# Kernel tuning notes

Measured on AMD Instinct MI355X. Metric: run time of the kernel, lower is better.

The kernel has to match this reference:

```python
import jax, jax.numpy as jnp
import numpy as np

B, J, D = 64, 512, 1024

def setup_inputs() -> dict:
    key = jax.random.key(0)
    k_x, k_m, k1, k2, k3 = jax.random.split(key, 5)
    x = jax.random.normal(k_x, (B, J, D), dtype=jnp.float32)
    mask = (jax.random.uniform(k_m, (B, J)) > 0.1).astype(jnp.float32)
    s1 = 1.0 / np.sqrt(D)
    W1 = jax.random.uniform(k1, (D, D), minval=-s1, maxval=s1, dtype=jnp.float32)
    b1 = jnp.zeros((D,), jnp.float32)
    W2 = jax.random.uniform(k2, (D, 1), minval=-s1, maxval=s1, dtype=jnp.float32)
    b2 = jnp.zeros((1,), jnp.float32)
    W3 = jax.random.uniform(k3, (D, 3), minval=-s1, maxval=s1, dtype=jnp.float32)
    b3 = jnp.zeros((3,), jnp.float32)
    return {"x": x, "mask": mask, "W1": W1, "b1": b1, "W2": W2, "b2": b2, "W3": W3, "b3": b3}

def reference(x, mask, W1, b1, W2, b2, W3, b3):
    # MLP attention scoring: linear1 -> tanh -> linear2 -> sigmoid
    h = jnp.tanh(jnp.einsum('bjd,de->bje', x, W1) + b1)          # [B,J,D]
    val = jax.nn.sigmoid(jnp.einsum('bjd,do->bjo', h, W2) + b2)  # [B,J,1]
    val = val * mask[:, :, None]                                  # mask out pads
    inv_sum = 1.0 / jnp.sum(val, axis=(1, 2))                     # [B]
    att_weights = val * inv_sum[:, None, None]                    # [B,J,1]
    pooled = jnp.einsum('bjk,bjm->bk', x, att_weights)            # [B,D]
    output_val = pooled @ W3 + b3                                 # [B,3]
    return output_val, att_weights
```

## Files before the change

kernel.cpp:

```cpp
#include <hip/hip_runtime.h>
#include <math.h>
#include <stdint.h>

#define B_ 64
#define J_ 512
#define D_ 1024

typedef __attribute__((ext_vector_type(8))) short short8;
typedef __attribute__((ext_vector_type(4))) float f32x4;

#define GLOBAL_AS __attribute__((address_space(1)))
#define LDS_AS    __attribute__((address_space(3)))

__device__ __forceinline__ void async16(const void* g, void* l) {
    __builtin_amdgcn_global_load_lds((const GLOBAL_AS uint32_t*)g,
                                     (LDS_AS uint32_t*)l, 16, 0, 0);
}

__device__ __forceinline__ float fast_tanh(float x) {
    return 1.0f - 2.0f / (1.0f + __expf(2.0f * x));
}

__device__ __forceinline__ unsigned short f2bf(float f) {
    uint32_t u = __builtin_bit_cast(uint32_t, f);
    u += 0x7fffu + ((u >> 16) & 1u);
    return (unsigned short)(u >> 16);
}

__device__ __forceinline__ uint32_t pk2(float a, float b) {
    return (uint32_t)f2bf(a) | ((uint32_t)f2bf(b) << 16);
}

__global__ __launch_bounds__(256) void prep_kernel(const float* __restrict__ W1,
                                                   unsigned short* __restrict__ W1t,
                                                   float* __restrict__ pooled) {
    __shared__ float t[32][33];
    const int b   = blockIdx.x;
    const int tid = threadIdx.x;
    if (b < 256) pooled[b * 256 + tid] = 0.f;
    const int bx = b & 31, by = b >> 5;
    const int tx = tid & 31, ty = tid >> 5;
    const int n = bx * 32 + tx;
    for (int i = ty; i < 32; i += 8)
        t[i][tx] = W1[(size_t)(by * 32 + i) * D_ + n];
    __syncthreads();
    const int k = by * 32 + tx;
    for (int i = ty; i < 32; i += 8)
        W1t[(size_t)(bx * 32 + i) * D_ + k] = f2bf(t[tx][i]);
}

__global__ __launch_bounds__(512, 4) void gemm_score_kernel(
    const float* __restrict__ x, const unsigned short* __restrict__ W1t,
    const float* __restrict__ b1, const float* __restrict__ W2,
    const float* __restrict__ b2, const float* __restrict__ mask,
    float* __restrict__ val_ws, float* __restrict__ pooled)
{
    __shared__ __align__(16) unsigned short ldsA[64 * 64];
    __shared__ __align__(16) unsigned short ldsB[512 * 64];

    const int tid  = threadIdx.x;
    const int wave = tid >> 6;
    const int l    = tid & 63;
    const int l15  = l & 15;
    const int kgrp = l >> 4;
    const int l7   = l & 7;
    const int r0   = blockIdx.x * 64;
    const int bb   = r0 >> 9;

    const int arow = tid >> 3;
    const int ach  = ((tid & 7) ^ (arow & 7)) << 3;
    const float* gAx = x + (size_t)(r0 + arow) * D_ + ach;

    const unsigned short* gB0 = W1t + (size_t)arow * D_ + ach;
    unsigned short* lB0 = ldsB + (wave << 9);

    int abase[2], bbase[2];
    #pragma unroll
    for (int ks = 0; ks < 2; ++ks) {
        const int swz = (((ks * 4 + kgrp) ^ l7) << 3);
        abase[ks] = l15 * 64 + swz;
        bbase[ks] = (wave * 64 + l15) * 64 + swz;
    }

    float pv[4][4];
    #pragma unroll
    for (int mi = 0; mi < 4; ++mi)
        #pragma unroll
        for (int r = 0; r < 4; ++r) pv[mi][r] = 0.f;

    uint4 curA;
    {
        const float4 p0 = *reinterpret_cast<const float4*>(gAx);
        const float4 p1 = *reinterpret_cast<const float4*>(gAx + 4);
        curA = (uint4){pk2(p0.x, p0.y), pk2(p0.z, p0.w),
                       pk2(p1.x, p1.y), pk2(p1.z, p1.w)};
    }

    #pragma unroll
    for (int n0 = 0; n0 < 2; ++n0) {
        f32x4 acc[4][4];
        #pragma unroll
        for (int mi = 0; mi < 4; ++mi)
            #pragma unroll
            for (int ni = 0; ni < 4; ++ni)
                acc[mi][ni] = (f32x4){0.f, 0.f, 0.f, 0.f};

        const size_t bofs = (size_t)n0 * 512 * D_;
        for (int k0 = 0; k0 < D_; k0 += 64) {
            *reinterpret_cast<uint4*>(ldsA + tid * 8) = curA;
            #pragma unroll
            for (int t = 0; t < 8; ++t)
                async16(gB0 + bofs + (size_t)t * 64 * D_ + k0, lB0 + t * 4096);
            __syncthreads();

            const int nk = (k0 == D_ - 64) ? 0 : k0 + 64;
            const float4 q0 = *reinterpret_cast<const float4*>(gAx + nk);
            const float4 q1 = *reinterpret_cast<const float4*>(gAx + nk + 4);

            #pragma unroll
            for (int ks = 0; ks < 2; ++ks) {
                const short8 a0 = *reinterpret_cast<const short8*>(ldsA + abase[ks]);
                const short8 a1 = *reinterpret_cast<const short8*>(ldsA + abase[ks] + 1024);
                const short8 a2 = *reinterpret_cast<const short8*>(ldsA + abase[ks] + 2048);
                const short8 a3 = *reinterpret_cast<const short8*>(ldsA + abase[ks] + 3072);
                #pragma unroll
                for (int ni = 0; ni < 4; ++ni) {
                    const short8 bv = *reinterpret_cast<const short8*>(
                        ldsB + bbase[ks] + ni * 1024);
                    acc[0][ni] = __builtin_amdgcn_mfma_f32_16x16x32_bf16(a0, bv, acc[0][ni], 0, 0, 0);
                    acc[1][ni] = __builtin_amdgcn_mfma_f32_16x16x32_bf16(a1, bv, acc[1][ni], 0, 0, 0);
                    acc[2][ni] = __builtin_amdgcn_mfma_f32_16x16x32_bf16(a2, bv, acc[2][ni], 0, 0, 0);
                    acc[3][ni] = __builtin_amdgcn_mfma_f32_16x16x32_bf16(a3, bv, acc[3][ni], 0, 0, 0);
                }
            }

            curA = (uint4){pk2(q0.x, q0.y), pk2(q0.z, q0.w),
                           pk2(q1.x, q1.y), pk2(q1.z, q1.w)};
            __syncthreads();
        }

        #pragma unroll
        for (int ni = 0; ni < 4; ++ni) {
            const int col = n0 * 512 + wave * 64 + ni * 16 + l15;
            const float b1v = b1[col];
            const float w2v = W2[col];
            #pragma unroll
            for (int mi = 0; mi < 4; ++mi)
                #pragma unroll
                for (int r = 0; r < 4; ++r) {
                    const float h = fast_tanh(acc[mi][ni][r] + b1v);
                    pv[mi][r] = fmaf(h, w2v, pv[mi][r]);
                }
        }
    }

    float* pv_part = reinterpret_cast<float*>(ldsB);
    float* vrow    = pv_part + 512;

    #pragma unroll
    for (int mi = 0; mi < 4; ++mi)
        #pragma unroll
        for (int r = 0; r < 4; ++r) {
            float s = pv[mi][r];
            s += __shfl_xor(s, 1);
            s += __shfl_xor(s, 2);
            s += __shfl_xor(s, 4);
            s += __shfl_xor(s, 8);
            if (l15 == 0) pv_part[wave * 64 + mi * 16 + kgrp * 4 + r] = s;
        }
    __syncthreads();
    if (tid < 64) {
        float s = b2[0];
        #pragma unroll
        for (int w = 0; w < 8; ++w) s += pv_part[w * 64 + tid];
        const float sg = 1.0f / (1.0f + __expf(-s));
        const float v = sg * mask[r0 + tid];
        val_ws[r0 + tid] = v;
        vrow[tid] = v;
    }
    __syncthreads();

    const int kc = tid << 1;
    float a0 = 0.f, a1 = 0.f;
    for (int row = 0; row < 64; ++row) {
        const float v = vrow[row];
        const float2 xv = *reinterpret_cast<const float2*>(
            x + (size_t)(r0 + row) * D_ + kc);
        a0 = fmaf(xv.x, v, a0);
        a1 = fmaf(xv.y, v, a1);
    }
    atomicAdd(&pooled[bb * D_ + kc], a0);
    atomicAdd(&pooled[bb * D_ + kc + 1], a1);
}

#define MT 64
#define KT 32
#define PAD 68

__global__ __launch_bounds__(256) void score_kernel_fp32(
    const float* __restrict__ x, const float* __restrict__ mask,
    const float* __restrict__ W1, const float* __restrict__ b1,
    const float* __restrict__ W2, const float* __restrict__ b2,
    float* __restrict__ val_ws, float* __restrict__ pooled)
{
    __shared__ float As[KT][PAD];
    __shared__ float Bs[KT][PAD];
    __shared__ float red[MT][17];
    __shared__ float vrow[MT];

    const int tid = threadIdx.x;
    const int tx = tid & 15;
    const int ty = tid >> 4;
    const int r0 = blockIdx.x * MT;
    const int b  = r0 >> 9;

    float pv[4] = {0.f, 0.f, 0.f, 0.f};

    for (int n0 = 0; n0 < D_; n0 += 64) {
        float acc[4][4];
        #pragma unroll
        for (int i = 0; i < 4; ++i)
            #pragma unroll
            for (int j = 0; j < 4; ++j) acc[i][j] = 0.f;

        for (int k0 = 0; k0 < D_; k0 += KT) {
            #pragma unroll
            for (int ll = 0; ll < 2; ++ll) {
                const int f   = tid + ll * 256;
                const int row = f >> 3;
                const int k4  = (f & 7) << 2;
                const float4 xv = *reinterpret_cast<const float4*>(
                    &x[(size_t)(r0 + row) * D_ + k0 + k4]);
                As[k4 + 0][row] = xv.x;
                As[k4 + 1][row] = xv.y;
                As[k4 + 2][row] = xv.z;
                As[k4 + 3][row] = xv.w;
            }
            #pragma unroll
            for (int ll = 0; ll < 2; ++ll) {
                const int f  = tid + ll * 256;
                const int k  = f >> 4;
                const int n4 = (f & 15) << 2;
                const float4 wv = *reinterpret_cast<const float4*>(
                    &W1[(size_t)(k0 + k) * D_ + n0 + n4]);
                *reinterpret_cast<float4*>(&Bs[k][n4]) = wv;
            }
            __syncthreads();
            #pragma unroll
            for (int kk = 0; kk < KT; ++kk) {
                const float4 a4 = *reinterpret_cast<const float4*>(&As[kk][ty << 2]);
                const float4 b4 = *reinterpret_cast<const float4*>(&Bs[kk][tx << 2]);
                const float av[4] = {a4.x, a4.y, a4.z, a4.w};
                const float bv[4] = {b4.x, b4.y, b4.z, b4.w};
                #pragma unroll
                for (int i = 0; i < 4; ++i)
                    #pragma unroll
                    for (int j = 0; j < 4; ++j)
                        acc[i][j] = fmaf(av[i], bv[j], acc[i][j]);
            }
            __syncthreads();
        }
        #pragma unroll
        for (int j = 0; j < 4; ++j) {
            const int col = n0 + (tx << 2) + j;
            const float b1v = b1[col];
            const float w2v = W2[col];
            #pragma unroll
            for (int i = 0; i < 4; ++i) {
                const float h = fast_tanh(acc[i][j] + b1v);
                pv[i] = fmaf(h, w2v, pv[i]);
            }
        }
    }

    #pragma unroll
    for (int i = 0; i < 4; ++i) red[(ty << 2) + i][tx] = pv[i];
    __syncthreads();

    if (tid < MT) {
        float s = 0.f;
        #pragma unroll
        for (int t = 0; t < 16; ++t) s += red[tid][t];
        const float z  = s + b2[0];
        const float sg = 1.0f / (1.0f + __expf(-z));
        const float v  = sg * mask[r0 + tid];
        val_ws[r0 + tid] = v;
        vrow[tid] = v;
    }
    __syncthreads();

    const int k = tid << 2;
    float a0 = 0.f, a1 = 0.f, a2 = 0.f, a3 = 0.f;
    for (int row = 0; row < MT; ++row) {
        const float v = vrow[row];
        const float4 xv = *reinterpret_cast<const float4*>(
            &x[(size_t)(r0 + row) * D_ + k]);
        a0 = fmaf(xv.x, v, a0);
        a1 = fmaf(xv.y, v, a1);
        a2 = fmaf(xv.z, v, a2);
        a3 = fmaf(xv.w, v, a3);
    }
    float* pb = &pooled[b * D_ + k];
    atomicAdd(pb + 0, a0);
    atomicAdd(pb + 1, a1);
    atomicAdd(pb + 2, a2);
    atomicAdd(pb + 3, a3);
}

__global__ __launch_bounds__(256) void finalize_kernel(
    const float* __restrict__ val_ws, const float* __restrict__ pooled,
    const float* __restrict__ W3, const float* __restrict__ b3,
    float* __restrict__ out)
{
    __shared__ float sred[256];
    const int b = blockIdx.x;
    const int tid = threadIdx.x;

    const float v0 = val_ws[b * J_ + tid];
    const float v1 = val_ws[b * J_ + 256 + tid];
    sred[tid] = v0 + v1;
    __syncthreads();
    for (int s = 128; s > 0; s >>= 1) {
        if (tid < s) sred[tid] += sred[tid + s];
        __syncthreads();
    }
    const float inv = 1.0f / sred[0];

    out[192 + b * J_ + tid]       = v0 * inv;
    out[192 + b * J_ + 256 + tid] = v1 * inv;

    const int k = tid << 2;
    float acc3[3] = {0.f, 0.f, 0.f};
    #pragma unroll
    for (int c = 0; c < 4; ++c) {
        const float p = pooled[b * D_ + k + c] * inv;
        acc3[0] = fmaf(p, W3[(k + c) * 3 + 0], acc3[0]);
        acc3[1] = fmaf(p, W3[(k + c) * 3 + 1], acc3[1]);
        acc3[2] = fmaf(p, W3[(k + c) * 3 + 2], acc3[2]);
    }
    for (int o = 0; o < 3; ++o) {
        __syncthreads();
        sred[tid] = acc3[o];
        __syncthreads();
        for (int s = 128; s > 0; s >>= 1) {
            if (tid < s) sred[tid] += sred[tid + s];
            __syncthreads();
        }
        if (tid == 0) out[b * 3 + o] = sred[0] + b3[o];
    }
}

extern "C" void kernel_launch(void* const* d_in, const int* in_sizes, int n_in,
                              void* d_out, int out_size, void* d_ws, size_t ws_size,
                              hipStream_t stream) {
    const float* x    = (const float*)d_in[0];
    const float* mask = (const float*)d_in[1];
    const float* W1   = (const float*)d_in[2];
    const float* b1   = (const float*)d_in[3];
    const float* W2   = (const float*)d_in[4];
    const float* b2   = (const float*)d_in[5];
    const float* W3   = (const float*)d_in[6];
    const float* b3   = (const float*)d_in[7];
    float* out = (float*)d_out;

    const size_t W1T_BYTES  = (size_t)D_ * D_ * 2;
    const size_t VAL_BYTES  = (size_t)B_ * J_ * 4;
    const size_t POOL_BYTES = (size_t)B_ * D_ * 4;
    const size_t NEED = W1T_BYTES + VAL_BYTES + POOL_BYTES;

    if (ws_size >= NEED) {
        unsigned short* W1t = (unsigned short*)d_ws;
        float* val_ws = (float*)((char*)d_ws + W1T_BYTES);
        float* pooled = (float*)((char*)d_ws + W1T_BYTES + VAL_BYTES);

        prep_kernel<<<1024, 256, 0, stream>>>(W1, W1t, pooled);
        gemm_score_kernel<<<512, 512, 0, stream>>>(x, W1t, b1, W2, b2, mask,
                                                   val_ws, pooled);
        finalize_kernel<<<B_, 256, 0, stream>>>(val_ws, pooled, W3, b3, out);
    } else {
        float* val_ws = (float*)d_ws;
        float* pooled = val_ws + B_ * J_;
        hipMemsetAsync(pooled, 0, POOL_BYTES, stream);
        score_kernel_fp32<<<(B_ * J_) / MT, 256, 0, stream>>>(
            x, mask, W1, b1, W2, b2, val_ws, pooled);
        finalize_kernel<<<B_, 256, 0, stream>>>(val_ws, pooled, W3, b3, out);
    }
}
```

Baseline: 308.1 us.

## Stream fp32 A tiles via async LDS loads and convert to bf16 after LDS read

The x tile is no longer loaded into registers, converted to bf16 and stored to LDS. It is now copied as fp32 straight into LDS with global_load_lds, using an XOR-swizzled layout. Each wave then reads fp32 from LDS and converts it with the hardware v_cvt_pk_bf16_f32 instruction just before the MFMAs. This removes the register staging and the software rounding. The cost is twice the LDS footprint and read traffic for A, repeated conversion work across waves, and the loss of the explicit register prefetch overlap for A.

```diff
diff --git a/kernel.cpp b/kernel.cpp
--- a/kernel.cpp
+++ b/kernel.cpp
@@ -27,8 +27,15 @@
     return (unsigned short)(u >> 16);
 }
 
-__device__ __forceinline__ uint32_t pk2(float a, float b) {
-    return (uint32_t)f2bf(a) | ((uint32_t)f2bf(b) << 16);
+__device__ __forceinline__ short8 cvt8(const f32x4 lo, const f32x4 hi) {
+    uint32_t w0, w1, w2, w3;
+    asm("v_cvt_pk_bf16_f32 %0, %1, %2" : "=v"(w0) : "v"(lo[0]), "v"(lo[1]));
+    asm("v_cvt_pk_bf16_f32 %0, %1, %2" : "=v"(w1) : "v"(lo[2]), "v"(lo[3]));
+    asm("v_cvt_pk_bf16_f32 %0, %1, %2" : "=v"(w2) : "v"(hi[0]), "v"(hi[1]));
+    asm("v_cvt_pk_bf16_f32 %0, %1, %2" : "=v"(w3) : "v"(hi[2]), "v"(hi[3]));
+    union { uint32_t u[4]; short8 s; } cv;
+    cv.u[0] = w0; cv.u[1] = w1; cv.u[2] = w2; cv.u[3] = w3;
+    return cv.s;
 }
 
 __global__ __launch_bounds__(256) void prep_kernel(const float* __restrict__ W1,
@@ -55,7 +62,7 @@
     const float* __restrict__ b2, const float* __restrict__ mask,
     float* __restrict__ val_ws, float* __restrict__ pooled)
 {
-    __shared__ __align__(16) unsigned short ldsA[64 * 64];
+    __shared__ __align__(16) float          ldsAf[64 * 64];
     __shared__ __align__(16) unsigned short ldsB[512 * 64];
 
     const int tid  = threadIdx.x;
@@ -67,20 +74,28 @@
     const int r0   = blockIdx.x * 64;
     const int bb   = r0 >> 9;
 
-    const int arow = tid >> 3;
-    const int ach  = ((tid & 7) ^ (arow & 7)) << 3;
-    const float* gAx = x + (size_t)(r0 + arow) * D_ + ach;
-
-    const unsigned short* gB0 = W1t + (size_t)arow * D_ + ach;
+    const int q0r = tid >> 4,          q0c = tid & 15;
+    const int q1r = (tid + 512) >> 4,  q1c = tid & 15;
+    const float* gA0 = x + (size_t)(r0 + q0r) * D_ + ((q0c ^ (q0r & 15)) << 2);
+    const float* gA1 = x + (size_t)(r0 + q1r) * D_ + ((q1c ^ (q1r & 15)) << 2);
+    float* lA0 = ldsAf + (wave << 8);
+    float* lA1 = lA0 + 2048;
+
+    const int brow = tid >> 3;
+    const int bch  = ((tid & 7) ^ (brow & 7)) << 3;
+    const unsigned short* gB0 = W1t + (size_t)brow * D_ + bch;
     unsigned short* lB0 = ldsB + (wave << 9);
 
-    int abase[2], bbase[2];
-    #pragma unroll
-    for (int ks = 0; ks < 2; ++ks) {
-        const int swz = (((ks * 4 + kgrp) ^ l7) << 3);
-        abase[ks] = l15 * 64 + swz;
-        bbase[ks] = (wave * 64 + l15) * 64 + swz;
-    }
+    int afo[4][2];
+    #pragma unroll
+    for (int mi = 0; mi < 4; ++mi)
+        #pragma unroll
+        for (int ks = 0; ks < 2; ++ks)
+            afo[mi][ks] = (mi * 16 + l15) * 64 + (((ks * 8 + kgrp * 2) ^ l15) << 2);
+    int bbase[2];
+    #pragma unroll
+    for (int ks = 0; ks < 2; ++ks)
+        bbase[ks] = (wave * 64 + l15) * 64 + (((ks * 4 + kgrp) ^ l7) << 3);
 
     float pv[4][4];
     #pragma unroll
@@ -88,15 +103,6 @@
         #pragma unroll
         for (int r = 0; r < 4; ++r) pv[mi][r] = 0.f;
 
-    uint4 curA;
-    {
-        const float4 p0 = *reinterpret_cast<const float4*>(gAx);
-        const float4 p1 = *reinterpret_cast<const float4*>(gAx + 4);
-        curA = (uint4){pk2(p0.x, p0.y), pk2(p0.z, p0.w),
-                       pk2(p1.x, p1.y), pk2(p1.z, p1.w)};
-    }
-
-    #pragma unroll
     for (int n0 = 0; n0 < 2; ++n0) {
         f32x4 acc[4][4];
         #pragma unroll
@@ -107,35 +113,31 @@
 
         const size_t bofs = (size_t)n0 * 512 * D_;
         for (int k0 = 0; k0 < D_; k0 += 64) {
-            *reinterpret_cast<uint4*>(ldsA + tid * 8) = curA;
+            async16(gA0 + k0, lA0);
+            async16(gA1 + k0, lA1);
             #pragma unroll
             for (int t = 0; t < 8; ++t)
                 async16(gB0 + bofs + (size_t)t * 64 * D_ + k0, lB0 + t * 4096);
             __syncthreads();
-
-            const int nk = (k0 == D_ - 64) ? 0 : k0 + 64;
-            const float4 q0 = *reinterpret_cast<const float4*>(gAx + nk);
-            const float4 q1 = *reinterpret_cast<const float4*>(gAx + nk + 4);
-
             #pragma unroll
             for (int ks = 0; ks < 2; ++ks) {
-                const short8 a0 = *reinterpret_cast<const short8*>(ldsA + abase[ks]);
-                const short8 a1 = *reinterpret_cast<const short8*>(ldsA + abase[ks] + 1024);
-                const short8 a2 = *reinterpret_cast<const short8*>(ldsA + abase[ks] + 2048);
-                const short8 a3 = *reinterpret_cast<const short8*>(ldsA + abase[ks] + 3072);
+                short8 a[4];
+                #pragma unroll
+                for (int mi = 0; mi < 4; ++mi) {
+                    const f32x4 lo = *reinterpret_cast<const f32x4*>(ldsAf + afo[mi][ks]);
+                    const f32x4 hi = *reinterpret_cast<const f32x4*>(ldsAf + (afo[mi][ks] ^ 4));
+                    a[mi] = cvt8(lo, hi);
+                }
                 #pragma unroll
                 for (int ni = 0; ni < 4; ++ni) {
                     const short8 bv = *reinterpret_cast<const short8*>(
                         ldsB + bbase[ks] + ni * 1024);
-                    acc[0][ni] = __builtin_amdgcn_mfma_f32_16x16x32_bf16(a0, bv, acc[0][ni], 0, 0, 0);
-                    acc[1][ni] = __builtin_amdgcn_mfma_f32_16x16x32_bf16(a1, bv, acc[1][ni], 0, 0, 0);
-                    acc[2][ni] = __builtin_amdgcn_mfma_f32_16x16x32_bf16(a2, bv, acc[2][ni], 0, 0, 0);
-                    acc[3][ni] = __builtin_amdgcn_mfma_f32_16x16x32_bf16(a3, bv, acc[3][ni], 0, 0, 0);
+                    acc[0][ni] = __builtin_amdgcn_mfma_f32_16x16x32_bf16(a[0], bv, acc[0][ni], 0, 0, 0);
+                    acc[1][ni] = __builtin_amdgcn_mfma_f32_16x16x32_bf16(a[1], bv, acc[1][ni], 0, 0, 0);
+                    acc[2][ni] = __builtin_amdgcn_mfma_f32_16x16x32_bf16(a[2], bv, acc[2][ni], 0, 0, 0);
+                    acc[3][ni] = __builtin_amdgcn_mfma_f32_16x16x32_bf16(a[3], bv, acc[3][ni], 0, 0, 0);
                 }
             }
-
-            curA = (uint4){pk2(q0.x, q0.y), pk2(q0.z, q0.w),
-                           pk2(q1.x, q1.y), pk2(q1.z, q1.w)};
             __syncthreads();
         }
 
```

After: 303.7 us. About the same (-1.4%).
